# Performance work log

Hardware: AMD Instinct MI355X
Metric: run time of the kernel (lower is better)

Reference implementation:

```python
import jax, jax.numpy as jnp
import numpy as np

D = 2048      # in_features == out_features == rank (forced by the module's shape algebra)
N = 8192
ALPHA = 16
SCALING = ALPHA / D
EPS = 1e-12   # F.normalize eps


def setup_inputs() -> dict:
    key = jax.random.key(0)
    kx, ka, kb, kd = jax.random.split(key, 4)
    x = jax.random.normal(kx, (N, D), dtype=jnp.float32)
    # Parameters per DoRALayer.__init__. Note: the original inits lora_B to zeros,
    # which makes the whole forward identically zero; we use small randn instead
    # so the baseline exercises non-trivial numerics (same math).
    lora_A = jax.random.normal(ka, (D, D), dtype=jnp.float32) * 0.01  # [rank, in]
    lora_B = jax.random.normal(kb, (D, D), dtype=jnp.float32) * 0.01  # [out, rank]
    magnitude = jnp.ones((D,), dtype=jnp.float32)                      # [out]
    direction = jax.random.normal(kd, (D, D), dtype=jnp.float32) * 0.01  # [out, rank]
    return {"x": x, "lora_A": lora_A, "lora_B": lora_B,
            "magnitude": magnitude, "direction": direction}


def reference(x, lora_A, lora_B, magnitude, direction):
    # W = lora_A.T @ lora_B.T  -> [in, out]
    W = jnp.einsum('ri,or->io', lora_A, lora_B)
    # F.linear(x, W) = x @ W.T  -> [N, in]
    lora_output = jnp.einsum('no,io->ni', x, W) * SCALING
    # torch.norm(magnitude): scalar L2 norm of the magnitude vector
    mag = jnp.linalg.norm(magnitude)
    # F.normalize(direction, p=2, dim=1) with eps clamp
    dnorm = jnp.sqrt(jnp.sum(direction * direction, axis=1, keepdims=True))
    dirn = direction / jnp.maximum(dnorm, EPS)
    # (direction @ lora_output.T).T  -> [N, out]
    dora_output = mag * jnp.einsum('or,nr->no', dirn, lora_output)
    return dora_output
```

## Files before the change

kernel.cpp:

```cpp
#include <hip/hip_runtime.h>

typedef unsigned short u16;
typedef unsigned int   u32;
typedef __attribute__((ext_vector_type(8))) __bf16 bf16x8;
typedef __attribute__((ext_vector_type(4))) float  f32x4;

#define D_DIM 2048
#define N_TOK 8192

__device__ __forceinline__ u16 f2bf(float f) {
  u32 u = __float_as_uint(f);
  u32 r = (u + 0x7fffu + ((u >> 16) & 1u)) >> 16;
  return (u16)r;
}

__device__ __forceinline__ void gl16(const void* g, void* l) {
  __builtin_amdgcn_global_load_lds((const __attribute__((address_space(1))) void*)g,
                                   (__attribute__((address_space(3))) void*)l,
                                   16, 0, 0);
}

__global__ __launch_bounds__(256) void cvt_f32_bf16(const float* __restrict__ in,
                                                    u16* __restrict__ out, int n4) {
  int idx = blockIdx.x * 256 + threadIdx.x;
  int stride = gridDim.x * 256;
  for (int i = idx; i < n4; i += stride) {
    float4 v = ((const float4*)in)[i];
    ushort4 o;
    o.x = f2bf(v.x); o.y = f2bf(v.y); o.z = f2bf(v.z); o.w = f2bf(v.w);
    ((ushort4*)out)[i] = o;
  }
}

__global__ __launch_bounds__(256) void normalize_rows(const float* __restrict__ dir,
                                                      u16* __restrict__ out) {
  const int row = blockIdx.x;
  const int tid = threadIdx.x;
  const float4* r = (const float4*)(dir + (size_t)row * D_DIM);
  float4 v0 = r[tid * 2 + 0];
  float4 v1 = r[tid * 2 + 1];
  float ss = v0.x*v0.x + v0.y*v0.y + v0.z*v0.z + v0.w*v0.w
           + v1.x*v1.x + v1.y*v1.y + v1.z*v1.z + v1.w*v1.w;
  #pragma unroll
  for (int off = 32; off > 0; off >>= 1) ss += __shfl_down(ss, off);
  __shared__ float red[4];
  __shared__ float invs;
  if ((tid & 63) == 0) red[tid >> 6] = ss;
  __syncthreads();
  if (tid == 0) {
    float t = red[0] + red[1] + red[2] + red[3];
    invs = 1.0f / fmaxf(sqrtf(t), 1e-12f);
  }
  __syncthreads();
  float inv = invs;
  ushort4 o0, o1;
  o0.x = f2bf(v0.x * inv); o0.y = f2bf(v0.y * inv);
  o0.z = f2bf(v0.z * inv); o0.w = f2bf(v0.w * inv);
  o1.x = f2bf(v1.x * inv); o1.y = f2bf(v1.y * inv);
  o1.z = f2bf(v1.z * inv); o1.w = f2bf(v1.w * inv);
  ushort4* ow = (ushort4*)(out + (size_t)row * D_DIM);
  ow[tid * 2 + 0] = o0;
  ow[tid * 2 + 1] = o1;
}

__global__ __launch_bounds__(256) void mag_scale_k(const float* __restrict__ m,
                                                   float* __restrict__ scale,
                                                   int n, float scaling) {
  const int tid = threadIdx.x;
  float ss = 0.0f;
  for (int i = tid; i < n / 4; i += 256) {
    float4 v = ((const float4*)m)[i];
    ss += v.x*v.x + v.y*v.y + v.z*v.z + v.w*v.w;
  }
  #pragma unroll
  for (int off = 32; off > 0; off >>= 1) ss += __shfl_down(ss, off);
  __shared__ float red[4];
  if ((tid & 63) == 0) red[tid >> 6] = ss;
  __syncthreads();
  if (tid == 0) {
    float t = red[0] + red[1] + red[2] + red[3];
    scale[0] = sqrtf(t) * scaling;
  }
}

template <int OUT_BF16>
__global__ __launch_bounds__(256)
void gemm_nt(const u16* __restrict__ A, const u16* __restrict__ B,
             void* __restrict__ Cv, int M, int Nn, int K,
             const float* __restrict__ scale_ptr) {
  __shared__ __align__(16) u16 lA[128 * 64];
  __shared__ __align__(16) u16 lB[128 * 64];
  const int tid  = threadIdx.x;
  const int lane = tid & 63;
  const int wave = tid >> 6;
  const int wr = wave >> 1, wc = wave & 1;
  const int row0 = blockIdx.y * 128, col0 = blockIdx.x * 128;

  const u16* Ag = A + (size_t)row0 * K;
  const u16* Bg = B + (size_t)col0 * K;

  f32x4 acc[4][4];
  #pragma unroll
  for (int i = 0; i < 4; ++i)
    #pragma unroll
    for (int j = 0; j < 4; ++j)
      acc[i][j] = (f32x4){0.0f, 0.0f, 0.0f, 0.0f};

  const int rsub = lane >> 3;
  const int sm   = lane & 7;

  for (int k0 = 0; k0 < K; k0 += 64) {
    #pragma unroll
    for (int j = 0; j < 4; ++j) {
      int c  = wave * 4 + j;
      int rt = c * 8 + rsub;
      int ssrc = sm ^ (rt & 7);
      gl16(Ag + (size_t)rt * K + k0 + ssrc * 8, &lA[c * 512 + lane * 8]);
      gl16(Bg + (size_t)rt * K + k0 + ssrc * 8, &lB[c * 512 + lane * 8]);
    }
    __syncthreads();

    #pragma unroll
    for (int ks = 0; ks < 2; ++ks) {
      bf16x8 af[4], bfr[4];
      #pragma unroll
      for (int mi = 0; mi < 4; ++mi) {
        int ra = wr * 64 + mi * 16 + (lane & 15);
        int sa = (ks * 4 + (lane >> 4)) ^ (ra & 7);
        af[mi] = *(const bf16x8*)&lA[ra * 64 + sa * 8];
        int rb = wc * 64 + mi * 16 + (lane & 15);
        int sb = (ks * 4 + (lane >> 4)) ^ (rb & 7);
        bfr[mi] = *(const bf16x8*)&lB[rb * 64 + sb * 8];
      }
      #pragma unroll
      for (int mi = 0; mi < 4; ++mi)
        #pragma unroll
        for (int ni = 0; ni < 4; ++ni)
          acc[mi][ni] = __builtin_amdgcn_mfma_f32_16x16x32_bf16(
              af[mi], bfr[ni], acc[mi][ni], 0, 0, 0);
    }
    __syncthreads();
  }

  float scl = scale_ptr ? scale_ptr[0] : 1.0f;
  const int orow = row0 + wr * 64 + (lane >> 4) * 4;
  const int ocol = col0 + wc * 64 + (lane & 15);
  #pragma unroll
  for (int mi = 0; mi < 4; ++mi) {
    #pragma unroll
    for (int ni = 0; ni < 4; ++ni) {
      #pragma unroll
      for (int r = 0; r < 4; ++r) {
        int gr = orow + mi * 16 + r;
        int gc = ocol + ni * 16;
        float v = acc[mi][ni][r] * scl;
        if (OUT_BF16) ((u16*)Cv)[(size_t)gr * Nn + gc] = f2bf(v);
        else          ((float*)Cv)[(size_t)gr * Nn + gc] = v;
      }
    }
  }
}

#define STG(tile, half) do {                                                   \
    const u16* G_ = ((half) < 2) ? (A + (size_t)(row0 + ((half)&1)*128) * K)   \
                                 : (B + (size_t)(col0 + ((half)&1)*128) * K);  \
    u16* L_ = &lds[(tile)&1][half][0];                                         \
    const int k0_ = (tile) << 6;                                               \
    { int idx = tid;       int rt = idx >> 3, sm2 = idx & 7;                   \
      gl16(G_ + (size_t)rt*K + k0_ + (sm2 ^ (rt&7))*8, L_ + idx*8); }          \
    { int idx = 512 + tid; int rt = idx >> 3, sm2 = idx & 7;                   \
      gl16(G_ + (size_t)rt*K + k0_ + (sm2 ^ (rt&7))*8, L_ + idx*8); }          \
  } while (0)

#define RDA(b, mi, ks) (*(const bf16x8*)&lds[b][wr][((mi)*16 + fr)*64 + ((((ks)*4 + fs) ^ (fr & 7)))*8])
#define RDB(b, ni, ks) (*(const bf16x8*)&lds[b][2 + ((wc*64 + (ni)*16 + fr) >> 7)][((wc*64 + (ni)*16 + fr) & 127)*64 + ((((ks)*4 + fs) ^ (fr & 7)))*8])
#define MFMA(a, bb, c) __builtin_amdgcn_mfma_f32_16x16x32_bf16(a, bb, c, 0, 0, 0)

template <int OUT_BF16>
__global__ __launch_bounds__(512, 2)
void gemm_nt8(const u16* __restrict__ A, const u16* __restrict__ B,
              void* __restrict__ Cv, int M, int Nn, int K,
              const float* __restrict__ scale_ptr) {
  __shared__ __align__(16) u16 lds[2][4][128 * 64];
  const int tid  = threadIdx.x;
  const int lane = tid & 63;
  const int wave = tid >> 6;
  const int wr = wave >> 2;
  const int wc = wave & 3;
  const int row0 = blockIdx.y * 256, col0 = blockIdx.x * 256;
  const int NT = K >> 6;
  const int fr = lane & 15, fs = lane >> 4;

  f32x4 acc[8][4];
  #pragma unroll
  for (int i = 0; i < 8; ++i)
    #pragma unroll
    for (int j = 0; j < 4; ++j)
      acc[i][j] = (f32x4){0.0f, 0.0f, 0.0f, 0.0f};

  STG(0, 0); STG(0, 1); STG(0, 2); STG(0, 3);
  if (NT > 1) {
    STG(1, 0); STG(1, 1); STG(1, 2); STG(1, 3);
    asm volatile("s_waitcnt vmcnt(8)" ::: "memory");
  } else {
    asm volatile("s_waitcnt vmcnt(0)" ::: "memory");
  }
  __builtin_amdgcn_s_barrier();

  for (int t = 0; t < NT; ++t) {
    const int b = t & 1;
    bf16x8 aF[8], bL[4], bH[4];

    #pragma unroll
    for (int mi = 0; mi < 4; ++mi) { aF[mi*2] = RDA(b, mi, 0); aF[mi*2+1] = RDA(b, mi, 1); }
    #pragma unroll
    for (int ni = 0; ni < 2; ++ni) { bL[ni*2] = RDB(b, ni, 0); bL[ni*2+1] = RDB(b, ni, 1); }
    __builtin_amdgcn_s_barrier();
    asm volatile("s_waitcnt lgkmcnt(0)");
    __builtin_amdgcn_s_setprio(1);
    #pragma unroll
    for (int mi = 0; mi < 4; ++mi)
      #pragma unroll
      for (int ni = 0; ni < 2; ++ni)
        #pragma unroll
        for (int ks = 0; ks < 2; ++ks)
          acc[mi][ni] = MFMA(aF[mi*2+ks], bL[ni*2+ks], acc[mi][ni]);
    __builtin_amdgcn_s_setprio(0);
    __builtin_amdgcn_s_barrier();

    #pragma unroll
    for (int ni = 0; ni < 2; ++ni) { bH[ni*2] = RDB(b, ni + 2, 0); bH[ni*2+1] = RDB(b, ni + 2, 1); }
    __builtin_amdgcn_s_barrier();
    asm volatile("s_waitcnt lgkmcnt(0)");
    __builtin_amdgcn_s_setprio(1);
    #pragma unroll
    for (int mi = 0; mi < 4; ++mi)
      #pragma unroll
      for (int ni = 0; ni < 2; ++ni)
        #pragma unroll
        for (int ks = 0; ks < 2; ++ks)
          acc[mi][ni + 2] = MFMA(aF[mi*2+ks], bH[ni*2+ks], acc[mi][ni + 2]);
    __builtin_amdgcn_s_setprio(0);
    __builtin_amdgcn_s_barrier();

    #pragma unroll
    for (int mi = 0; mi < 4; ++mi) { aF[mi*2] = RDA(b, mi + 4, 0); aF[mi*2+1] = RDA(b, mi + 4, 1); }
    if (t + 2 < NT) { STG(t + 2, 2); STG(t + 2, 3); }
    __builtin_amdgcn_s_barrier();
    asm volatile("s_waitcnt lgkmcnt(0)");
    __builtin_amdgcn_s_setprio(1);
    #pragma unroll
    for (int mi = 0; mi < 4; ++mi)
      #pragma unroll
      for (int ni = 0; ni < 2; ++ni)
        #pragma unroll
        for (int ks = 0; ks < 2; ++ks)
          acc[mi + 4][ni + 2] = MFMA(aF[mi*2+ks], bH[ni*2+ks], acc[mi + 4][ni + 2]);
    __builtin_amdgcn_s_setprio(0);
    __builtin_amdgcn_s_barrier();

    if (t + 2 < NT) { STG(t + 2, 0); STG(t + 2, 1); }
    __builtin_amdgcn_s_barrier();
    asm volatile("s_waitcnt lgkmcnt(0)");
    __builtin_amdgcn_s_setprio(1);
    #pragma unroll
    for (int mi = 0; mi < 4; ++mi)
      #pragma unroll
      for (int ni = 0; ni < 2; ++ni)
        #pragma unroll
        for (int ks = 0; ks < 2; ++ks)
          acc[mi + 4][ni] = MFMA(aF[mi*2+ks], bL[ni*2+ks], acc[mi + 4][ni]);
    __builtin_amdgcn_s_setprio(0);
    if (t < NT - 2) asm volatile("s_waitcnt vmcnt(8)" ::: "memory");
    else            asm volatile("s_waitcnt vmcnt(0)" ::: "memory");
    __builtin_amdgcn_s_barrier();
  }

  float scl = scale_ptr ? scale_ptr[0] : 1.0f;
  #pragma unroll
  for (int mi = 0; mi < 8; ++mi) {
    #pragma unroll
    for (int ni = 0; ni < 4; ++ni) {
      #pragma unroll
      for (int r = 0; r < 4; ++r) {
        int gr = row0 + wr * 128 + mi * 16 + fs * 4 + r;
        int gc = col0 + wc * 64 + ni * 16 + fr;
        float v = acc[mi][ni][r] * scl;
        if (OUT_BF16) ((u16*)Cv)[(size_t)gr * Nn + gc] = f2bf(v);
        else          ((float*)Cv)[(size_t)gr * Nn + gc] = v;
      }
    }
  }
}

extern "C" void kernel_launch(void* const* d_in, const int* in_sizes, int n_in,
                              void* d_out, int out_size, void* d_ws, size_t ws_size,
                              hipStream_t stream) {
  const float* x    = (const float*)d_in[0];
  const float* lorA = (const float*)d_in[1];
  const float* lorB = (const float*)d_in[2];
  const float* mag  = (const float*)d_in[3];
  const float* dir  = (const float*)d_in[4];
  float* out = (float*)d_out;

  char* ws = (char*)d_ws;
  u16*   xb  = (u16*)(ws);
  u16*   Ab  = (u16*)(ws + 33554432);
  u16*   Bb  = (u16*)(ws + 41943040);
  u16*   Db  = (u16*)(ws + 50331648);
  u16*   CT  = (u16*)(ws + 58720256);
  float* scl = (float*)(ws + 67108864);
  u16*   WfT = Db;

  cvt_f32_bf16<<<2048, 256, 0, stream>>>(x,    xb, N_TOK * D_DIM / 4);
  cvt_f32_bf16<<<1024, 256, 0, stream>>>(lorA, Ab, D_DIM * D_DIM / 4);
  cvt_f32_bf16<<<1024, 256, 0, stream>>>(lorB, Bb, D_DIM * D_DIM / 4);
  normalize_rows<<<D_DIM, 256, 0, stream>>>(dir, Db);
  mag_scale_k<<<1, 256, 0, stream>>>(mag, scl, D_DIM, 16.0f / 2048.0f);

  gemm_nt<1><<<dim3(D_DIM / 128, D_DIM / 128), 256, 0, stream>>>(
      Db, Ab, CT, D_DIM, D_DIM, D_DIM, nullptr);
  gemm_nt<1><<<dim3(D_DIM / 128, D_DIM / 128), 256, 0, stream>>>(
      CT, Bb, WfT, D_DIM, D_DIM, D_DIM, nullptr);
  gemm_nt8<0><<<dim3(D_DIM / 256, N_TOK / 256), 512, 0, stream>>>(
      xb, WfT, out, N_TOK, D_DIM, D_DIM, scl);
}
```

Measured before the change: 312.9 us.

## Split-K small weight GEMMs, fuse prep kernels, and remap big GEMM tiles per XCD

The two 2048^3 weight GEMMs now run split-K by 4, so each launches 1024 workgroups instead of 256. The bf16 partials go to workspace and a separate kernel sums them. The two lora conversions are merged into one launch, mag-norm is folded into the direction-normalize kernel, and the x conversion moves after the weight GEMMs so its workspace can hold the partials. The big GEMM remaps block IDs so each XCD gets a contiguous run of tiles for L2 locality. Costs are extra partial-sum traffic, the reduce launches, and bf16 rounding of the partials.

```diff
diff --git a/kernel.cpp b/kernel.cpp
--- a/kernel.cpp
+++ b/kernel.cpp
@@ -12,6 +12,9 @@
   u32 u = __float_as_uint(f);
   u32 r = (u + 0x7fffu + ((u >> 16) & 1u)) >> 16;
   return (u16)r;
+}
+__device__ __forceinline__ float b2f(u16 h) {
+  return __uint_as_float(((u32)h) << 16);
 }
 
 __device__ __forceinline__ void gl16(const void* g, void* l) {
@@ -32,10 +35,51 @@
   }
 }
 
-__global__ __launch_bounds__(256) void normalize_rows(const float* __restrict__ dir,
-                                                      u16* __restrict__ out) {
+__global__ __launch_bounds__(256) void cvt2_f32_bf16(const float* __restrict__ inA,
+                                                     u16* __restrict__ outA,
+                                                     const float* __restrict__ inB,
+                                                     u16* __restrict__ outB, int n4) {
+  const int half = gridDim.x >> 1;
+  const bool lo = (int)blockIdx.x < half;
+  const float* in = lo ? inA : inB;
+  u16* out = lo ? outA : outB;
+  int bid = lo ? blockIdx.x : blockIdx.x - half;
+  int idx = bid * 256 + threadIdx.x;
+  int stride = half * 256;
+  for (int i = idx; i < n4; i += stride) {
+    float4 v = ((const float4*)in)[i];
+    ushort4 o;
+    o.x = f2bf(v.x); o.y = f2bf(v.y); o.z = f2bf(v.z); o.w = f2bf(v.w);
+    ((ushort4*)out)[i] = o;
+  }
+}
+
+__global__ __launch_bounds__(256) void norm_mag(const float* __restrict__ dir,
+                                                u16* __restrict__ out,
+                                                const float* __restrict__ mag,
+                                                float* __restrict__ scale) {
+  __shared__ float red[4];
+  __shared__ float invs;
+  const int tid = threadIdx.x;
+
+  if (blockIdx.x == D_DIM) {
+    float ss = 0.0f;
+    for (int i = tid; i < D_DIM / 4; i += 256) {
+      float4 v = ((const float4*)mag)[i];
+      ss += v.x*v.x + v.y*v.y + v.z*v.z + v.w*v.w;
+    }
+    #pragma unroll
+    for (int off = 32; off > 0; off >>= 1) ss += __shfl_down(ss, off);
+    if ((tid & 63) == 0) red[tid >> 6] = ss;
+    __syncthreads();
+    if (tid == 0) {
+      float t = red[0] + red[1] + red[2] + red[3];
+      scale[0] = sqrtf(t) * (16.0f / 2048.0f);
+    }
+    return;
+  }
+
   const int row = blockIdx.x;
-  const int tid = threadIdx.x;
   const float4* r = (const float4*)(dir + (size_t)row * D_DIM);
   float4 v0 = r[tid * 2 + 0];
   float4 v1 = r[tid * 2 + 1];
@@ -43,8 +87,6 @@
            + v1.x*v1.x + v1.y*v1.y + v1.z*v1.z + v1.w*v1.w;
   #pragma unroll
   for (int off = 32; off > 0; off >>= 1) ss += __shfl_down(ss, off);
-  __shared__ float red[4];
-  __shared__ float invs;
   if ((tid & 63) == 0) red[tid >> 6] = ss;
   __syncthreads();
   if (tid == 0) {
@@ -63,31 +105,9 @@
   ow[tid * 2 + 1] = o1;
 }
 
-__global__ __launch_bounds__(256) void mag_scale_k(const float* __restrict__ m,
-                                                   float* __restrict__ scale,
-                                                   int n, float scaling) {
-  const int tid = threadIdx.x;
-  float ss = 0.0f;
-  for (int i = tid; i < n / 4; i += 256) {
-    float4 v = ((const float4*)m)[i];
-    ss += v.x*v.x + v.y*v.y + v.z*v.z + v.w*v.w;
-  }
-  #pragma unroll
-  for (int off = 32; off > 0; off >>= 1) ss += __shfl_down(ss, off);
-  __shared__ float red[4];
-  if ((tid & 63) == 0) red[tid >> 6] = ss;
-  __syncthreads();
-  if (tid == 0) {
-    float t = red[0] + red[1] + red[2] + red[3];
-    scale[0] = sqrtf(t) * scaling;
-  }
-}
-
-template <int OUT_BF16>
 __global__ __launch_bounds__(256)
-void gemm_nt(const u16* __restrict__ A, const u16* __restrict__ B,
-             void* __restrict__ Cv, int M, int Nn, int K,
-             const float* __restrict__ scale_ptr) {
+void gemm_nt_sk(const u16* __restrict__ A, const u16* __restrict__ B,
+                u16* __restrict__ P, int M, int Nn, int K, int klen) {
   __shared__ __align__(16) u16 lA[128 * 64];
   __shared__ __align__(16) u16 lB[128 * 64];
   const int tid  = threadIdx.x;
@@ -95,6 +115,7 @@
   const int wave = tid >> 6;
   const int wr = wave >> 1, wc = wave & 1;
   const int row0 = blockIdx.y * 128, col0 = blockIdx.x * 128;
+  const int kbeg = blockIdx.z * klen;
 
   const u16* Ag = A + (size_t)row0 * K;
   const u16* Bg = B + (size_t)col0 * K;
@@ -109,7 +130,7 @@
   const int rsub = lane >> 3;
   const int sm   = lane & 7;
 
-  for (int k0 = 0; k0 < K; k0 += 64) {
+  for (int k0 = kbeg; k0 < kbeg + klen; k0 += 64) {
     #pragma unroll
     for (int j = 0; j < 4; ++j) {
       int c  = wave * 4 + j;
@@ -142,22 +163,34 @@
     __syncthreads();
   }
 
-  float scl = scale_ptr ? scale_ptr[0] : 1.0f;
+  u16* Pz = P + (size_t)blockIdx.z * M * Nn;
   const int orow = row0 + wr * 64 + (lane >> 4) * 4;
   const int ocol = col0 + wc * 64 + (lane & 15);
   #pragma unroll
-  for (int mi = 0; mi < 4; ++mi) {
-    #pragma unroll
-    for (int ni = 0; ni < 4; ++ni) {
-      #pragma unroll
-      for (int r = 0; r < 4; ++r) {
-        int gr = orow + mi * 16 + r;
-        int gc = ocol + ni * 16;
-        float v = acc[mi][ni][r] * scl;
-        if (OUT_BF16) ((u16*)Cv)[(size_t)gr * Nn + gc] = f2bf(v);
-        else          ((float*)Cv)[(size_t)gr * Nn + gc] = v;
-      }
-    }
+  for (int mi = 0; mi < 4; ++mi)
+    #pragma unroll
+    for (int ni = 0; ni < 4; ++ni)
+      #pragma unroll
+      for (int r = 0; r < 4; ++r)
+        Pz[(size_t)(orow + mi * 16 + r) * Nn + (ocol + ni * 16)] = f2bf(acc[mi][ni][r]);
+}
+
+__global__ __launch_bounds__(256) void reduce4_bf16(const u16* __restrict__ P,
+                                                    u16* __restrict__ out,
+                                                    int n4, int slice4) {
+  int idx = blockIdx.x * 256 + threadIdx.x;
+  int stride = gridDim.x * 256;
+  for (int i = idx; i < n4; i += stride) {
+    ushort4 a = ((const ushort4*)P)[i];
+    ushort4 b = ((const ushort4*)P)[i + slice4];
+    ushort4 c = ((const ushort4*)P)[i + 2 * slice4];
+    ushort4 d = ((const ushort4*)P)[i + 3 * slice4];
+    ushort4 o;
+    o.x = f2bf(b2f(a.x) + b2f(b.x) + b2f(c.x) + b2f(d.x));
+    o.y = f2bf(b2f(a.y) + b2f(b.y) + b2f(c.y) + b2f(d.y));
+    o.z = f2bf(b2f(a.z) + b2f(b.z) + b2f(c.z) + b2f(d.z));
+    o.w = f2bf(b2f(a.w) + b2f(b.w) + b2f(c.w) + b2f(d.w));
+    ((ushort4*)out)[i] = o;
   }
 }
 
@@ -187,7 +220,15 @@
   const int wave = tid >> 6;
   const int wr = wave >> 2;
   const int wc = wave & 3;
-  const int row0 = blockIdx.y * 256, col0 = blockIdx.x * 256;
+
+  const int nwg = gridDim.x * gridDim.y;
+  const int lid = blockIdx.y * gridDim.x + blockIdx.x;
+  const int q = nwg >> 3, r = nwg & 7;
+  const int xcd = lid & 7, i8 = lid >> 3;
+  const int wg = (xcd < r ? xcd * (q + 1) : r * (q + 1) + (xcd - r) * q) + i8;
+  const int by = wg / gridDim.x, bx = wg - by * gridDim.x;
+
+  const int row0 = by * 256, col0 = bx * 256;
   const int NT = K >> 6;
   const int fr = lane & 15, fs = lane >> 4;
 
@@ -305,6 +346,7 @@
 
   char* ws = (char*)d_ws;
   u16*   xb  = (u16*)(ws);
+  u16*   Pp  = xb;
   u16*   Ab  = (u16*)(ws + 33554432);
   u16*   Bb  = (u16*)(ws + 41943040);
   u16*   Db  = (u16*)(ws + 50331648);
@@ -312,16 +354,17 @@
   float* scl = (float*)(ws + 67108864);
   u16*   WfT = Db;
 
-  cvt_f32_bf16<<<2048, 256, 0, stream>>>(x,    xb, N_TOK * D_DIM / 4);
-  cvt_f32_bf16<<<1024, 256, 0, stream>>>(lorA, Ab, D_DIM * D_DIM / 4);
-  cvt_f32_bf16<<<1024, 256, 0, stream>>>(lorB, Bb, D_DIM * D_DIM / 4);
-  normalize_rows<<<D_DIM, 256, 0, stream>>>(dir, Db);
-  mag_scale_k<<<1, 256, 0, stream>>>(mag, scl, D_DIM, 16.0f / 2048.0f);
-
-  gemm_nt<1><<<dim3(D_DIM / 128, D_DIM / 128), 256, 0, stream>>>(
-      Db, Ab, CT, D_DIM, D_DIM, D_DIM, nullptr);
-  gemm_nt<1><<<dim3(D_DIM / 128, D_DIM / 128), 256, 0, stream>>>(
-      CT, Bb, WfT, D_DIM, D_DIM, D_DIM, nullptr);
+  cvt2_f32_bf16<<<2048, 256, 0, stream>>>(lorA, Ab, lorB, Bb, D_DIM * D_DIM / 4);
+  norm_mag<<<D_DIM + 1, 256, 0, stream>>>(dir, Db, mag, scl);
+
+  gemm_nt_sk<<<dim3(16, 16, 4), 256, 0, stream>>>(Db, Ab, Pp, D_DIM, D_DIM, D_DIM, 512);
+  reduce4_bf16<<<1024, 256, 0, stream>>>(Pp, CT, D_DIM * D_DIM / 4, D_DIM * D_DIM / 4);
+
+  gemm_nt_sk<<<dim3(16, 16, 4), 256, 0, stream>>>(CT, Bb, Pp, D_DIM, D_DIM, D_DIM, 512);
+  reduce4_bf16<<<1024, 256, 0, stream>>>(Pp, WfT, D_DIM * D_DIM / 4, D_DIM * D_DIM / 4);
+
+  cvt_f32_bf16<<<2048, 256, 0, stream>>>(x, xb, N_TOK * D_DIM / 4);
+
   gemm_nt8<0><<<dim3(D_DIM / 256, N_TOK / 256), 512, 0, stream>>>(
       xb, WfT, out, N_TOK, D_DIM, D_DIM, scl);
 }
```

After: 311.6 us. About the same (-0.4%).
